# Optimization experiments

Measured on AMD Instinct MI355X. Metric: run time of the kernel, lower is better.

The kernel has to match this reference:

```python
import jax, jax.numpy as jnp
import numpy as np

B, T, E, H = 4, 512, 1024, 16
D = E // H  # 64
EPS = 1e-5  # torch LayerNorm default


def _ln(x, g, b):
    m = jnp.mean(x, axis=-1, keepdims=True)
    v = jnp.mean(jnp.square(x - m), axis=-1, keepdims=True)
    return (x - m) * jax.lax.rsqrt(v + EPS) * g + b


def _multihead(x, wq, wk, wv, g, b, mask):
    # x: [B,T,E]; wq/wk/wv: [H,E,D]; g,b: [H,D]; mask: [T,T] bool (causal)
    q = jnp.einsum('bte,hed->bhtd', x, wq)
    k = jnp.einsum('bte,hed->bhtd', x, wk)
    v = jnp.einsum('bte,hed->bhtd', x, wv)
    aff = jnp.einsum('bhtd,bhsd->bhts', q, k)  # NOTE: no 1/sqrt(d) scaling, as in source
    aff = jnp.where(mask, aff, -jnp.inf)
    p = jax.nn.softmax(aff, axis=-1)
    o = jnp.einsum('bhts,bhsd->bhtd', p, v)
    o = _ln(o, g[None, :, None, :], b[None, :, None, :])  # per-head LayerNorm over D
    o = o.transpose(0, 2, 1, 3).reshape(B, T, E)  # concat heads
    return x + o


def _ff(x, w1, b1, w2, b2, g, bb):
    h = jnp.maximum(jnp.einsum('bte,ef->btf', x, w1) + b1, 0.0)
    h = jnp.einsum('btf,fe->bte', h, w2) + b2
    h = _ln(h, g, bb)
    return x + h


def setup_inputs() -> dict:
    key = jax.random.key(0)
    ks = jax.random.split(key, 8)
    s = 0.02
    return {
        'x': jax.random.normal(ks[0], (B, T, E), jnp.float32),
        'mh_wq': jax.random.normal(ks[1], (5, H, E, D), jnp.float32) * s,
        'mh_wk': jax.random.normal(ks[2], (5, H, E, D), jnp.float32) * s,
        'mh_wv': jax.random.normal(ks[3], (5, H, E, D), jnp.float32) * s,
        'mh_g': jnp.ones((5, H, D), jnp.float32),
        'mh_b': jnp.zeros((5, H, D), jnp.float32),
        'ff_w1': jax.random.normal(ks[4], (4, E, 4 * E), jnp.float32) * s,
        'ff_b1': jnp.zeros((4, 4 * E), jnp.float32),
        'ff_w2': jax.random.normal(ks[5], (4, 4 * E, E), jnp.float32) * s,
        'ff_b2': jnp.zeros((4, E), jnp.float32),
        'ff_g': jnp.ones((4, E), jnp.float32),
        'ff_bb': jnp.zeros((4, E), jnp.float32),
        'lt_w': jax.random.normal(ks[6], (2 * E, E), jnp.float32) * s,
        'lt_b': jnp.zeros((E,), jnp.float32),
    }


def reference(x, mh_wq, mh_wk, mh_wv, mh_g, mh_b,
              ff_w1, ff_b1, ff_w2, ff_b2, ff_g, ff_bb, lt_w, lt_b):
    mask = jnp.tril(jnp.ones((T, T), dtype=bool))

    def mh(i, y):
        return _multihead(y, mh_wq[i], mh_wk[i], mh_wv[i], mh_g[i], mh_b[i], mask)

    def ff(i, y):
        return _ff(y, ff_w1[i], ff_b1[i], ff_w2[i], ff_b2[i], ff_g[i], ff_bb[i])

    def decoder(y):  # MultiHeadwithEncoder + FeedForward (param sets 4 / 3)
        return ff(3, mh(4, y))

    # head_one branch
    out_one = decoder(mh(0, x))
    # encoder branch: 3 EncoderBlocks (MultiHead + FeedForward each)
    out_two = x
    for i in range(3):
        out_two = ff(i, mh(1 + i, out_two))
    out_two = decoder(out_two)

    out = jnp.concatenate([out_one, out_two], axis=-1)
    out = jnp.einsum('btf,fe->bte', out, lt_w) + lt_b
    # input; the result is identical each time, so computing it once is faithful.
    return out
```

## Files before the change

### kernel.cpp

```cpp
#include <hip/hip_runtime.h>
#include <math.h>

#define Bb 4
#define Tt 512
#define Ee 1024
#define Hh 16
#define Dd 64
#define Ff 4096
#define Mm (Bb*Tt)
static constexpr float EPS = 1e-5f;

typedef __attribute__((ext_vector_type(4))) float f32x4;
typedef _Float16 f16;
typedef __attribute__((ext_vector_type(8))) _Float16 f16x8;

__device__ __forceinline__ void gload16(const void* g, void* l) {
  __builtin_amdgcn_global_load_lds(
      (const __attribute__((address_space(1))) unsigned int*)g,
      (__attribute__((address_space(3))) unsigned int*)l, 16, 0, 0);
}

__global__ __launch_bounds__(256)
void gemm_f16_128(const f16* __restrict__ A, const f16* __restrict__ W,
                  const float* __restrict__ bias,
                  f16* __restrict__ C, int ldc, int K)
{
  __shared__ f16 AS[128][32], BS[128][32];
  const int tid = threadIdx.x;
  const int lane = tid & 63, w = tid >> 6;
  const int wr = w >> 1, wc = w & 1;
  const int lhi = lane >> 4, llo = lane & 15;
  const int n0 = blockIdx.x * 128, m0 = blockIdx.y * 128;
  const int s_row = tid >> 2, s_ko = (tid & 3) * 8;

  f32x4 acc[4][4] = {};

  for (int k0 = 0; k0 < K; k0 += 32) {
#pragma unroll
    for (int i = 0; i < 2; ++i) {
      const int row = s_row + i * 64;
      gload16(&A[(size_t)(m0 + row) * K + k0 + s_ko], &AS[row][s_ko]);
      gload16(&W[(size_t)(n0 + row) * K + k0 + s_ko], &BS[row][s_ko]);
    }
    __syncthreads();
    f16x8 af[4], bf[4];
#pragma unroll
    for (int f = 0; f < 4; ++f) {
      af[f] = *(const f16x8*)&AS[wr * 64 + f * 16 + llo][lhi * 8];
      bf[f] = *(const f16x8*)&BS[wc * 64 + f * 16 + llo][lhi * 8];
    }
#pragma unroll
    for (int m = 0; m < 4; ++m)
#pragma unroll
      for (int n = 0; n < 4; ++n)
        acc[m][n] = __builtin_amdgcn_mfma_f32_16x16x32_f16(af[m], bf[n], acc[m][n], 0, 0, 0);
    __syncthreads();
  }

#pragma unroll
  for (int n = 0; n < 4; ++n) {
    const int col = n0 + wc * 64 + n * 16 + llo;
    const float bv = bias[col];
#pragma unroll
    for (int m = 0; m < 4; ++m) {
      const int rbase = m0 + wr * 64 + m * 16 + lhi * 4;
#pragma unroll
      for (int j = 0; j < 4; ++j) {
        float v = fmaxf(acc[m][n][j] + bv, 0.f);
        C[(size_t)(rbase + j) * ldc + col] = (f16)v;
      }
    }
  }
}

template<bool CONCAT>
__global__ __launch_bounds__(256)
void gemm_f16_1p(const f16* __restrict__ A, const f16* __restrict__ A2,
                 const f16* __restrict__ W,
                 float* __restrict__ Cf, float* __restrict__ Cf1,
                 int ldc, int K)
{
  __shared__ f16 AS[2][64][32], BS[2][128][32];
  const int tid = threadIdx.x;
  const int lane = tid & 63, w = tid >> 6;
  const int wr = w >> 1, wc = w & 1;
  const int lhi = lane >> 4, llo = lane & 15;
  const int n0 = blockIdx.x * 128;
  const int m0 = blockIdx.y * 64;
  const int half = K >> 1;
  const int kbeg = blockIdx.z * half;
  const int nt = half / 32;
  if (blockIdx.z == 1) Cf = Cf1;

  const int s_row = tid >> 2, s_ko = (tid & 3) * 8;

  auto stage = [&](int k0, int buf) {
    const int gk = k0 + s_ko;
    const f16* s = A;
    size_t g;
    if (CONCAT) {
      if (gk < Ee) { g = (size_t)(m0 + s_row) * Ee + gk; }
      else { g = (size_t)(m0 + s_row) * Ee + (gk - Ee); s = A2; }
    } else {
      g = (size_t)(m0 + s_row) * K + gk;
    }
    gload16(&s[g], &AS[buf][s_row][s_ko]);
#pragma unroll
    for (int i = 0; i < 2; ++i)
      gload16(&W[(size_t)(n0 + s_row + i * 64) * K + gk], &BS[buf][s_row + i * 64][s_ko]);
  };

  f32x4 acc[2][4] = {};
  stage(kbeg, 0);
  __syncthreads();
  int cur = 0;
  for (int t = 0; t < nt; ++t) {
    if (t + 1 < nt) stage(kbeg + (t + 1) * 32, cur ^ 1);
    f16x8 af[2], bf[4];
#pragma unroll
    for (int m = 0; m < 2; ++m)
      af[m] = *(const f16x8*)&AS[cur][wr * 32 + m * 16 + llo][lhi * 8];
#pragma unroll
    for (int n = 0; n < 4; ++n)
      bf[n] = *(const f16x8*)&BS[cur][wc * 64 + n * 16 + llo][lhi * 8];
#pragma unroll
    for (int m = 0; m < 2; ++m)
#pragma unroll
      for (int n = 0; n < 4; ++n)
        acc[m][n] = __builtin_amdgcn_mfma_f32_16x16x32_f16(af[m], bf[n], acc[m][n], 0, 0, 0);
    __syncthreads();
    cur ^= 1;
  }

#pragma unroll
  for (int n = 0; n < 4; ++n) {
    const int col = n0 + wc * 64 + n * 16 + llo;
#pragma unroll
    for (int m = 0; m < 2; ++m) {
      const int rbase = m0 + wr * 32 + m * 16 + lhi * 4;
#pragma unroll
      for (int j = 0; j < 4; ++j)
        Cf[(size_t)(rbase + j) * ldc + col] = acc[m][n][j];
    }
  }
}

__global__ __launch_bounds__(256)
void gemm_qkv(const f16* __restrict__ Ah_g, const f16* __restrict__ Al_g,
              const f16* __restrict__ Wh, const f16* __restrict__ Wl,
              f16* __restrict__ Qh, f16* __restrict__ Ql,
              f16* __restrict__ Kh, f16* __restrict__ Kl,
              f16* __restrict__ Vv)
{
  __shared__ f16 AhS[2][64][32], AlS[2][64][32];
  __shared__ f16 BhS[2][128][32], BlS[2][128][32];
  const int tid = threadIdx.x;
  const int lane = tid & 63, w = tid >> 6;
  const int wr = w >> 1, wc = w & 1;
  const int lhi = lane >> 4, llo = lane & 15;
  const int sec = blockIdx.x >> 3;
  const bool three = (sec < 2);
  const int n0 = (blockIdx.x & 7) * 128;
  Wh += (size_t)sec << 20;
  Wl += (size_t)sec << 20;
  const int m0 = blockIdx.y * 64;
  const int s_row = tid >> 2, s_ko = (tid & 3) * 8;

  auto stage = [&](int k0, int buf) {
    const size_t g = (size_t)(m0 + s_row) * Ee + k0 + s_ko;
    gload16(&Ah_g[g], &AhS[buf][s_row][s_ko]);
    if (three) gload16(&Al_g[g], &AlS[buf][s_row][s_ko]);
#pragma unroll
    for (int i = 0; i < 2; ++i) {
      size_t gb = (size_t)(n0 + s_row + i * 64) * Ee + k0 + s_ko;
      gload16(&Wh[gb], &BhS[buf][s_row + i * 64][s_ko]);
      if (three) gload16(&Wl[gb], &BlS[buf][s_row + i * 64][s_ko]);
    }
  };

  f32x4 acc[2][4] = {};
  stage(0, 0);
  __syncthreads();
  int cur = 0;
  for (int t = 0; t < Ee / 32; ++t) {
    if (t + 1 < Ee / 32) stage((t + 1) * 32, cur ^ 1);
    f16x8 ah[2], bh[4];
#pragma unroll
    for (int m = 0; m < 2; ++m)
      ah[m] = *(const f16x8*)&AhS[cur][wr * 32 + m * 16 + llo][lhi * 8];
#pragma unroll
    for (int n = 0; n < 4; ++n)
      bh[n] = *(const f16x8*)&BhS[cur][wc * 64 + n * 16 + llo][lhi * 8];
    if (three) {
      f16x8 al[2], bl[4];
#pragma unroll
      for (int m = 0; m < 2; ++m)
        al[m] = *(const f16x8*)&AlS[cur][wr * 32 + m * 16 + llo][lhi * 8];
#pragma unroll
      for (int n = 0; n < 4; ++n)
        bl[n] = *(const f16x8*)&BlS[cur][wc * 64 + n * 16 + llo][lhi * 8];
#pragma unroll
      for (int m = 0; m < 2; ++m)
#pragma unroll
        for (int n = 0; n < 4; ++n) {
          acc[m][n] = __builtin_amdgcn_mfma_f32_16x16x32_f16(ah[m], bh[n], acc[m][n], 0, 0, 0);
          acc[m][n] = __builtin_amdgcn_mfma_f32_16x16x32_f16(ah[m], bl[n], acc[m][n], 0, 0, 0);
          acc[m][n] = __builtin_amdgcn_mfma_f32_16x16x32_f16(al[m], bh[n], acc[m][n], 0, 0, 0);
        }
    } else {
#pragma unroll
      for (int m = 0; m < 2; ++m)
#pragma unroll
        for (int n = 0; n < 4; ++n)
          acc[m][n] = __builtin_amdgcn_mfma_f32_16x16x32_f16(ah[m], bh[n], acc[m][n], 0, 0, 0);
    }
    __syncthreads();
    cur ^= 1;
  }

#pragma unroll
  for (int n = 0; n < 4; ++n) {
    const int col = n0 + wc * 64 + n * 16 + llo;
#pragma unroll
    for (int m = 0; m < 2; ++m) {
      const int rbase = m0 + wr * 32 + m * 16 + lhi * 4;
#pragma unroll
      for (int j = 0; j < 4; ++j) {
        const float v = acc[m][n][j];
        const size_t idx = (size_t)(rbase + j) * Ee + col;
        if (sec == 0) {
          f16 h = (f16)v;
          Qh[idx] = h;
          Ql[idx] = (f16)(v - (float)h);
        } else if (sec == 1) {
          f16 h = (f16)v;
          Kh[idx] = h;
          Kl[idx] = (f16)(v - (float)h);
        } else {
          Vv[idx] = (f16)v;
        }
      }
    }
  }
}

__global__ __launch_bounds__(256)
void attn_ms(const f16* __restrict__ Qh_g, const f16* __restrict__ Ql_g,
             const f16* __restrict__ Kh_g, const f16* __restrict__ Kl_g,
             const f16* __restrict__ Vv_g, float* __restrict__ O)
{
  __shared__ f16 Ksh[64][72], Ksl[64][72];
  __shared__ f16 Vs[64][72];
  __shared__ f16 Pw[4][16][72];
  const int tid = threadIdx.x;
  const int lane = tid & 63, w = tid >> 6;
  const int lhi = lane >> 4, llo = lane & 15;
  const int q0 = blockIdx.x * 64;
  const int bh = blockIdx.y;
  const size_t base = (size_t)(bh >> 4) * Tt * Ee + (size_t)(bh & 15) * Dd;

  f16x8 qfh[2], qfl[2];
#pragma unroll
  for (int ks = 0; ks < 2; ++ks) {
    const size_t qoff = base + (size_t)(q0 + w * 16 + llo) * Ee + ks * 32 + lhi * 8;
    qfh[ks] = *(const f16x8*)&Qh_g[qoff];
    qfl[ks] = *(const f16x8*)&Ql_g[qoff];
  }

  f32x4 oacc[4] = {};
  float m_run[4], l_run[4];
#pragma unroll
  for (int j = 0; j < 4; ++j) { m_run[j] = -INFINITY; l_run[j] = 0.f; }

  for (int s0 = 0; s0 <= q0; s0 += 64) {
#pragma unroll
    for (int pass = 0; pass < 2; ++pass) {
      int c = tid + 256 * pass;
      int row = c >> 3, d0 = (c & 7) * 8;
      const size_t g = base + (size_t)(s0 + row) * Ee + d0;
      f16x8 kh = *(const f16x8*)&Kh_g[g];
      f16x8 kl = *(const f16x8*)&Kl_g[g];
      f16x8 vf = *(const f16x8*)&Vv_g[g];
      *(f16x8*)&Ksh[row][d0] = kh;
      *(f16x8*)&Ksl[row][d0] = kl;
#pragma unroll
      for (int j = 0; j < 8; ++j) Vs[d0 + j][row] = vf[j];
    }
    __syncthreads();

    f32x4 sacc[4] = {};
#pragma unroll
    for (int ks = 0; ks < 2; ++ks)
#pragma unroll
      for (int n = 0; n < 4; ++n) {
        f16x8 kfh = *(const f16x8*)&Ksh[n * 16 + llo][ks * 32 + lhi * 8];
        f16x8 kfl = *(const f16x8*)&Ksl[n * 16 + llo][ks * 32 + lhi * 8];
        sacc[n] = __builtin_amdgcn_mfma_f32_16x16x32_f16(qfh[ks], kfh, sacc[n], 0, 0, 0);
        sacc[n] = __builtin_amdgcn_mfma_f32_16x16x32_f16(qfh[ks], kfl, sacc[n], 0, 0, 0);
        sacc[n] = __builtin_amdgcn_mfma_f32_16x16x32_f16(qfl[ks], kfh, sacc[n], 0, 0, 0);
      }

    if (s0 == q0) {
#pragma unroll
      for (int n = 0; n < 4; ++n)
#pragma unroll
        for (int j = 0; j < 4; ++j)
          if (n * 16 + llo > w * 16 + lhi * 4 + j) sacc[n][j] = -INFINITY;
    }

    float scj[4];
#pragma unroll
    for (int j = 0; j < 4; ++j) {
      float mt = fmaxf(fmaxf(sacc[0][j], sacc[1][j]), fmaxf(sacc[2][j], sacc[3][j]));
#pragma unroll
      for (int off = 1; off < 16; off <<= 1) mt = fmaxf(mt, __shfl_xor(mt, off));
      float mn = fmaxf(m_run[j], mt);
      scj[j] = __expf(m_run[j] - mn);
      m_run[j] = mn;
      float rs = 0.f;
#pragma unroll
      for (int n = 0; n < 4; ++n) {
        float pp = __expf(sacc[n][j] - mn);
        sacc[n][j] = pp;
        rs += pp;
      }
#pragma unroll
      for (int off = 1; off < 16; off <<= 1) rs += __shfl_xor(rs, off);
      l_run[j] = l_run[j] * scj[j] + rs;
    }

#pragma unroll
    for (int n = 0; n < 4; ++n)
#pragma unroll
      for (int j = 0; j < 4; ++j)
        Pw[w][lhi * 4 + j][n * 16 + llo] = (f16)sacc[n][j];
#pragma unroll
    for (int df = 0; df < 4; ++df)
#pragma unroll
      for (int j = 0; j < 4; ++j)
        oacc[df][j] *= scj[j];

#pragma unroll
    for (int ks = 0; ks < 2; ++ks) {
      f16x8 pf = *(const f16x8*)&Pw[w][llo][ks * 32 + lhi * 8];
#pragma unroll
      for (int df = 0; df < 4; ++df) {
        f16x8 vfr = *(const f16x8*)&Vs[df * 16 + llo][ks * 32 + lhi * 8];
        oacc[df] = __builtin_amdgcn_mfma_f32_16x16x32_f16(pf, vfr, oacc[df], 0, 0, 0);
      }
    }
    __syncthreads();
  }

#pragma unroll
  for (int j = 0; j < 4; ++j) {
    float inv = 1.f / l_run[j];
#pragma unroll
    for (int df = 0; df < 4; ++df)
      O[base + (size_t)(q0 + w * 16 + lhi * 4 + j) * Ee + df * 16 + llo] =
          oacc[df][j] * inv;
  }
}

__global__ __launch_bounds__(256)
void attn_ln_res(const float* __restrict__ O, const float* Yin,
                 const float* __restrict__ g, const float* __restrict__ bta,
                 float* Yout, f16* __restrict__ Yh, f16* __restrict__ Yl)
{
  const int tid = threadIdx.x;
  const int w = (blockIdx.x << 2) + (tid >> 6);
  const int lane = tid & 63;
  const int m = w >> 4;
  const int h = w & 15;
  const size_t idx = (size_t)m * Ee + h * Dd + lane;
  float x = O[idx];
  float s = x, s2 = x * x;
#pragma unroll
  for (int off = 1; off < 64; off <<= 1) {
    s  += __shfl_xor(s, off);
    s2 += __shfl_xor(s2, off);
  }
  float mean = s * (1.f / 64.f);
  float var  = s2 * (1.f / 64.f) - mean * mean;
  float inv  = rsqrtf(var + EPS);
  float r = Yin[idx] + (x - mean) * inv * g[h * Dd + lane] + bta[h * Dd + lane];
  Yout[idx] = r;
  f16 hh = (f16)r;
  Yh[idx] = hh;
  Yl[idx] = (f16)(r - (float)hh);
}

__global__ __launch_bounds__(256)
void ff_ln_res(const float* __restrict__ T0, const float* __restrict__ T1,
               const float* __restrict__ b2,
               const float* Yin, const float* __restrict__ g,
               const float* __restrict__ bb,
               float* Yout, f16* __restrict__ Yh, f16* __restrict__ Yl)
{
  __shared__ float red[8];
  const int m = blockIdx.x;
  const int tid = threadIdx.x;
  const size_t basep = (size_t)m * Ee;
  float4 xa = *(const float4*)&T0[basep + (tid << 2)];
  float4 xb = *(const float4*)&T1[basep + (tid << 2)];
  float4 bv2 = *(const float4*)&b2[tid << 2];
  float xv[4] = {xa.x + xb.x + bv2.x, xa.y + xb.y + bv2.y,
                 xa.z + xb.z + bv2.z, xa.w + xb.w + bv2.w};
  float s  = xv[0] + xv[1] + xv[2] + xv[3];
  float s2 = xv[0]*xv[0] + xv[1]*xv[1] + xv[2]*xv[2] + xv[3]*xv[3];
#pragma unroll
  for (int off = 1; off < 64; off <<= 1) {
    s  += __shfl_xor(s, off);
    s2 += __shfl_xor(s2, off);
  }
  const int wid = tid >> 6;
  if ((tid & 63) == 0) { red[wid] = s; red[4 + wid] = s2; }
  __syncthreads();
  s  = red[0] + red[1] + red[2] + red[3];
  s2 = red[4] + red[5] + red[6] + red[7];
  float mean = s * (1.f / Ee);
  float var  = s2 * (1.f / Ee) - mean * mean;
  float inv  = rsqrtf(var + EPS);
  float4 y  = *(const float4*)&Yin[basep + (tid << 2)];
  float4 gg = *(const float4*)&g[tid << 2];
  float4 bv = *(const float4*)&bb[tid << 2];
  float gga[4] = {gg.x, gg.y, gg.z, gg.w};
  float bva[4] = {bv.x, bv.y, bv.z, bv.w};
  float ya[4] = {y.x, y.y, y.z, y.w};
  float o[4];
#pragma unroll
  for (int j = 0; j < 4; ++j) {
    o[j] = ya[j] + (xv[j] - mean) * inv * gga[j] + bva[j];
    f16 hh = (f16)o[j];
    Yh[basep + (tid << 2) + j] = hh;
    Yl[basep + (tid << 2) + j] = (f16)(o[j] - (float)hh);
  }
  *(float4*)&Yout[basep + (tid << 2)] = *(float4*)o;
}

__global__ __launch_bounds__(256)
void add2_bias(const float* __restrict__ p0, const float* __restrict__ p1,
               const float* __restrict__ b, float* __restrict__ out)
{
  const size_t i = ((size_t)blockIdx.x * 256 + threadIdx.x) * 4;
  const int col = (int)(i & (Ee - 1));
  float4 a = *(const float4*)&p0[i];
  float4 c = *(const float4*)&p1[i];
  float4 bb = *(const float4*)&b[col];
  float4 o;
  o.x = a.x + c.x + bb.x; o.y = a.y + c.y + bb.y;
  o.z = a.z + c.z + bb.z; o.w = a.w + c.w + bb.w;
  *(float4*)&out[i] = o;
}

__global__ __launch_bounds__(256)
void split_act2(const float* __restrict__ in,
                f16* __restrict__ oh1, f16* __restrict__ ol1,
                f16* __restrict__ oh2, f16* __restrict__ ol2)
{
  const size_t nb = gridDim.x >> 1;
  size_t bid = blockIdx.x;
  f16 *oh, *ol;
  if (bid < nb) { oh = oh1; ol = ol1; }
  else { bid -= nb; oh = oh2; ol = ol2; }
  const size_t i = (bid * 256 + threadIdx.x) * 4;
  float4 v = *(const float4*)&in[i];
  float f[4] = {v.x, v.y, v.z, v.w};
#pragma unroll
  for (int j = 0; j < 4; ++j) {
    f16 h = (f16)f[j];
    oh[i + j] = h;
    ol[i + j] = (f16)(f[j] - (float)h);
  }
}

__device__ __forceinline__ void cvtT_tile(const float* in, f16* outp,
                                          int R, int C, int tx, int ty, int tid)
{
  __shared__ float tile[64][33];
  const int c0 = tx * 32, r0 = ty * 64;
  const int r = tid >> 2, c8 = (tid & 3) * 8;
  const float* src = &in[(size_t)(r0 + r) * C + c0 + c8];
  float4 a = *(const float4*)src;
  float4 b = *(const float4*)(src + 4);
  tile[r][c8 + 0] = a.x; tile[r][c8 + 1] = a.y;
  tile[r][c8 + 2] = a.z; tile[r][c8 + 3] = a.w;
  tile[r][c8 + 4] = b.x; tile[r][c8 + 5] = b.y;
  tile[r][c8 + 6] = b.z; tile[r][c8 + 7] = b.w;
  __syncthreads();
  const int oc = tid >> 3, rr = (tid & 7) * 8;
  f16x8 o;
#pragma unroll
  for (int j = 0; j < 8; ++j) o[j] = (f16)tile[rr + j][oc];
  *(f16x8*)&outp[(size_t)(c0 + oc) * R + r0 + rr] = o;
}

__global__ __launch_bounds__(256)
void cvtT_f16(const float* __restrict__ in, f16* __restrict__ outp, int R, int C)
{
  const int nx = C >> 5;
  cvtT_tile(in, outp, R, C, blockIdx.x % nx, blockIdx.x / nx, threadIdx.x);
}

__global__ __launch_bounds__(256)
void cvtT_ff(const float* __restrict__ w1, const float* __restrict__ w2,
             f16* __restrict__ o1, f16* __restrict__ o2)
{
  constexpr int NT1 = (Ff / 32) * (Ee / 64);
  int id = blockIdx.x;
  const float* in; f16* outp; int R, C;
  if (id < NT1) { in = w1; outp = o1; R = Ee; C = Ff; }
  else { id -= NT1; in = w2; outp = o2; R = Ff; C = Ee; }
  const int nx = C >> 5;
  cvtT_tile(in, outp, R, C, id % nx, id / nx, threadIdx.x);
}

__global__ __launch_bounds__(256)
void cvtT_qkv(const float* __restrict__ wq, const float* __restrict__ wk,
              const float* __restrict__ wv, f16* __restrict__ out_h,
              f16* __restrict__ out_l)
{
  __shared__ float tile[64][33];
  const int z = blockIdx.z, sec = z >> 4, hh = z & 15;
  const float* in = (sec == 0) ? wq : (sec == 1) ? wk : wv;
  const size_t zi = (size_t)hh * Ee * Dd;
  const size_t zo = ((size_t)sec << 20) + (size_t)hh * Ee * Dd;
  const int c0 = blockIdx.x * 32, r0 = blockIdx.y * 64;
  const int tid = threadIdx.x;
  const int r = tid >> 2, c8 = (tid & 3) * 8;
  const float* src = &in[zi + (size_t)(r0 + r) * Dd + c0 + c8];
  float4 a = *(const float4*)src;
  float4 b = *(const float4*)(src + 4);
  tile[r][c8 + 0] = a.x; tile[r][c8 + 1] = a.y;
  tile[r][c8 + 2] = a.z; tile[r][c8 + 3] = a.w;
  tile[r][c8 + 4] = b.x; tile[r][c8 + 5] = b.y;
  tile[r][c8 + 6] = b.z; tile[r][c8 + 7] = b.w;
  __syncthreads();
  const int oc = tid >> 3, rr = (tid & 7) * 8;
  f16x8 oh, ol;
#pragma unroll
  for (int j = 0; j < 8; ++j) {
    float f = tile[rr + j][oc];
    f16 h = (f16)f;
    oh[j] = h;
    ol[j] = (f16)(f - (float)h);
  }
  const size_t ob = zo + (size_t)(c0 + oc) * Ee + r0 + rr;
  *(f16x8*)&out_h[ob] = oh;
  *(f16x8*)&out_l[ob] = ol;
}

extern "C" void kernel_launch(void* const* d_in, const int* in_sizes, int n_in,
                              void* d_out, int out_size, void* d_ws, size_t ws_size,
                              hipStream_t stream)
{
  const float* x     = (const float*)d_in[0];
  const float* mh_wq = (const float*)d_in[1];
  const float* mh_wk = (const float*)d_in[2];
  const float* mh_wv = (const float*)d_in[3];
  const float* mh_g  = (const float*)d_in[4];
  const float* mh_b  = (const float*)d_in[5];
  const float* ff_w1 = (const float*)d_in[6];
  const float* ff_b1 = (const float*)d_in[7];
  const float* ff_w2 = (const float*)d_in[8];
  const float* ff_b2 = (const float*)d_in[9];
  const float* ff_g  = (const float*)d_in[10];
  const float* ff_bb = (const float*)d_in[11];
  const float* lt_w  = (const float*)d_in[12];
  const float* lt_b  = (const float*)d_in[13];
  float* out = (float*)d_out;

  const size_t ME = (size_t)Mm * Ee;
  char* p = (char*)d_ws;
  auto alloc = [&](size_t bytes) { void* r = (void*)p; p += (bytes + 255) & ~(size_t)255; return r; };
  float* bufA  = (float*)alloc(ME * 4);
  f16*   bufAh = (f16*)alloc(ME * 2);
  f16*   bufAl = (f16*)alloc(ME * 2);
  float* bufB  = (float*)alloc(ME * 4);
  f16*   bufBh = (f16*)alloc(ME * 2);
  f16*   bufBl = (f16*)alloc(ME * 2);
  f16*   wt_h  = (f16*)alloc((size_t)Ff * Ee * 2);
  f16*   wt_l  = (f16*)alloc((size_t)Ff * Ee * 2);
  float* reg   = (float*)alloc((size_t)10 * 1024 * 1024 * 4);
  f16*   qh_   = (f16*)reg;
  f16*   ql_   = qh_ + ME;
  f16*   kh_   = qh_ + 2 * ME;
  f16*   kl_   = qh_ + 3 * ME;
  f16*   vv_   = qh_ + 4 * ME;
  float* ob    = reg + 5 * 1024 * 1024;
  f16*   hid   = (f16*)reg;
  float* tmp   = reg + 8 * 1024 * 1024;

  auto mh = [&](int i, const float* srcF, const f16* srcH, const f16* srcL,
                float* dstF, f16* dstH, f16* dstL) {
    const size_t wo = (size_t)i * Hh * Ee * Dd;
    cvtT_qkv<<<dim3(Dd / 32, Ee / 64, 48), 256, 0, stream>>>(
        mh_wq + wo, mh_wk + wo, mh_wv + wo, wt_h, wt_l);
    gemm_qkv<<<dim3(24, Mm / 64), 256, 0, stream>>>(
        srcH, srcL, wt_h, wt_l, qh_, ql_, kh_, kl_, vv_);
    attn_ms<<<dim3(Tt / 64, Bb * Hh), 256, 0, stream>>>(qh_, ql_, kh_, kl_, vv_, ob);
    attn_ln_res<<<dim3(Mm * Hh / 4), 256, 0, stream>>>(
        ob, srcF, mh_g + (size_t)i * Hh * Dd, mh_b + (size_t)i * Hh * Dd, dstF, dstH, dstL);
  };
  auto ff = [&](int i, const float* srcF, const f16* srcH,
                float* dstF, f16* dstH, f16* dstL, float* tmp1) {
    cvtT_ff<<<dim3((Ff / 32) * (Ee / 64) + (Ee / 32) * (Ff / 64)), 256, 0, stream>>>(
        ff_w1 + (size_t)i * Ee * Ff, ff_w2 + (size_t)i * Ff * Ee, wt_h, wt_l);
    gemm_f16_128<<<dim3(Ff / 128, Mm / 128), 256, 0, stream>>>(
        srcH, wt_h, ff_b1 + (size_t)i * Ff, hid, Ff, Ee);
    gemm_f16_1p<false><<<dim3(Ee / 128, Mm / 64, 2), 256, 0, stream>>>(
        hid, nullptr, wt_l, tmp, tmp1, Ee, Ff);
    ff_ln_res<<<dim3(Mm), 256, 0, stream>>>(
        tmp, tmp1, ff_b2 + (size_t)i * Ee,
        srcF, ff_g + (size_t)i * Ee, ff_bb + (size_t)i * Ee, dstF, dstH, dstL);
  };

  split_act2<<<dim3(2 * ME / 1024), 256, 0, stream>>>(x, bufAh, bufAl, bufBh, bufBl);

  mh(0, x, bufAh, bufAl, bufA, bufAh, bufAl);
  mh(4, bufA, bufAh, bufAl, bufA, bufAh, bufAl);
  ff(3, bufA, bufAh, bufA, bufAh, bufAl, bufB);

  mh(1, x, bufBh, bufBl, bufB, bufBh, bufBl);
  ff(0, bufB, bufBh, bufB, bufBh, bufBl, bufA);
  mh(2, bufB, bufBh, bufBl, bufB, bufBh, bufBl);
  ff(1, bufB, bufBh, bufB, bufBh, bufBl, bufA);
  mh(3, bufB, bufBh, bufBl, bufB, bufBh, bufBl);
  ff(2, bufB, bufBh, bufB, bufBh, bufBl, bufA);
  mh(4, bufB, bufBh, bufBl, bufB, bufBh, bufBl);
  ff(3, bufB, bufBh, bufB, bufBh, bufBl, bufA);

  cvtT_f16<<<dim3((Ee / 32) * (2 * Ee / 64)), 256, 0, stream>>>(lt_w, wt_h, 2 * Ee, Ee);
  gemm_f16_1p<true><<<dim3(Ee / 128, Mm / 64, 2), 256, 0, stream>>>(
      bufAh, bufBh, wt_h, bufA, bufB, Ee, 2 * Ee);
  add2_bias<<<dim3(ME / 1024), 256, 0, stream>>>(bufA, bufB, lt_b, out);
}
```

Baseline: 1.002 ms.

## Triple-buffer LDS staging in GEMM kernels with partial vmcnt waits

Result: slower. 1.152 ms (+15.0%).

```diff
diff --git a/kernel.cpp b/kernel.cpp
--- a/kernel.cpp
+++ b/kernel.cpp
@@ -19,13 +19,17 @@
       (const __attribute__((address_space(1))) unsigned int*)g,
       (__attribute__((address_space(3))) unsigned int*)l, 16, 0, 0);
 }
+__device__ __forceinline__ void wait_vm6() { asm volatile("s_waitcnt vmcnt(6)" ::: "memory"); }
+__device__ __forceinline__ void wait_vm4() { asm volatile("s_waitcnt vmcnt(4)" ::: "memory"); }
+__device__ __forceinline__ void wait_vm3() { asm volatile("s_waitcnt vmcnt(3)" ::: "memory"); }
+__device__ __forceinline__ void wait_vm0() { asm volatile("s_waitcnt vmcnt(0)" ::: "memory"); }
 
 __global__ __launch_bounds__(256)
 void gemm_f16_128(const f16* __restrict__ A, const f16* __restrict__ W,
                   const float* __restrict__ bias,
                   f16* __restrict__ C, int ldc, int K)
 {
-  __shared__ f16 AS[128][32], BS[128][32];
+  __shared__ f16 AS[3][128][32], BS[3][128][32];
   const int tid = threadIdx.x;
   const int lane = tid & 63, w = tid >> 6;
   const int wr = w >> 1, wc = w & 1;
@@ -33,28 +37,39 @@
   const int n0 = blockIdx.x * 128, m0 = blockIdx.y * 128;
   const int s_row = tid >> 2, s_ko = (tid & 3) * 8;
 
-  f32x4 acc[4][4] = {};
-
-  for (int k0 = 0; k0 < K; k0 += 32) {
+  auto stage = [&](int k0, int buf) {
 #pragma unroll
     for (int i = 0; i < 2; ++i) {
       const int row = s_row + i * 64;
-      gload16(&A[(size_t)(m0 + row) * K + k0 + s_ko], &AS[row][s_ko]);
-      gload16(&W[(size_t)(n0 + row) * K + k0 + s_ko], &BS[row][s_ko]);
-    }
-    __syncthreads();
+      gload16(&A[(size_t)(m0 + row) * K + k0 + s_ko], &AS[buf][row][s_ko]);
+      gload16(&W[(size_t)(n0 + row) * K + k0 + s_ko], &BS[buf][row][s_ko]);
+    }
+  };
+
+  f32x4 acc[4][4] = {};
+  const int nt = K / 32;
+  stage(0, 0);
+  stage(32, 1);
+  wait_vm4();
+  __builtin_amdgcn_s_barrier();
+  for (int t = 0; t < nt; ++t) {
+    const int cur = t % 3;
+    if (t + 2 < nt) stage((t + 2) * 32, (t + 2) % 3);
     f16x8 af[4], bf[4];
 #pragma unroll
     for (int f = 0; f < 4; ++f) {
-      af[f] = *(const f16x8*)&AS[wr * 64 + f * 16 + llo][lhi * 8];
-      bf[f] = *(const f16x8*)&BS[wc * 64 + f * 16 + llo][lhi * 8];
+      af[f] = *(const f16x8*)&AS[cur][wr * 64 + f * 16 + llo][lhi * 8];
+      bf[f] = *(const f16x8*)&BS[cur][wc * 64 + f * 16 + llo][lhi * 8];
     }
 #pragma unroll
     for (int m = 0; m < 4; ++m)
 #pragma unroll
       for (int n = 0; n < 4; ++n)
         acc[m][n] = __builtin_amdgcn_mfma_f32_16x16x32_f16(af[m], bf[n], acc[m][n], 0, 0, 0);
-    __syncthreads();
+    if (t + 1 < nt) {
+      if (t + 2 < nt) wait_vm4(); else wait_vm0();
+      __builtin_amdgcn_s_barrier();
+    }
   }
 
 #pragma unroll
@@ -80,7 +95,7 @@
                  float* __restrict__ Cf, float* __restrict__ Cf1,
                  int ldc, int K)
 {
-  __shared__ f16 AS[2][64][32], BS[2][128][32];
+  __shared__ f16 AS[3][64][32], BS[3][128][32];
   const int tid = threadIdx.x;
   const int lane = tid & 63, w = tid >> 6;
   const int wr = w >> 1, wc = w & 1;
@@ -112,10 +127,12 @@
 
   f32x4 acc[2][4] = {};
   stage(kbeg, 0);
-  __syncthreads();
-  int cur = 0;
+  stage(kbeg + 32, 1);
+  wait_vm3();
+  __builtin_amdgcn_s_barrier();
   for (int t = 0; t < nt; ++t) {
-    if (t + 1 < nt) stage(kbeg + (t + 1) * 32, cur ^ 1);
+    const int cur = t % 3;
+    if (t + 2 < nt) stage(kbeg + (t + 2) * 32, (t + 2) % 3);
     f16x8 af[2], bf[4];
 #pragma unroll
     for (int m = 0; m < 2; ++m)
@@ -128,8 +145,10 @@
 #pragma unroll
       for (int n = 0; n < 4; ++n)
         acc[m][n] = __builtin_amdgcn_mfma_f32_16x16x32_f16(af[m], bf[n], acc[m][n], 0, 0, 0);
-    __syncthreads();
-    cur ^= 1;
+    if (t + 1 < nt) {
+      if (t + 2 < nt) wait_vm3(); else wait_vm0();
+      __builtin_amdgcn_s_barrier();
+    }
   }
 
 #pragma unroll
@@ -152,8 +171,8 @@
               f16* __restrict__ Kh, f16* __restrict__ Kl,
               f16* __restrict__ Vv)
 {
-  __shared__ f16 AhS[2][64][32], AlS[2][64][32];
-  __shared__ f16 BhS[2][128][32], BlS[2][128][32];
+  __shared__ f16 AhS[3][64][32], AlS[3][64][32];
+  __shared__ f16 BhS[3][128][32], BlS[3][128][32];
   const int tid = threadIdx.x;
   const int lane = tid & 63, w = tid >> 6;
   const int wr = w >> 1, wc = w & 1;
@@ -177,13 +196,17 @@
       if (three) gload16(&Wl[gb], &BlS[buf][s_row + i * 64][s_ko]);
     }
   };
+  auto wait_vmL = [&]() { if (three) wait_vm6(); else wait_vm3(); };
 
   f32x4 acc[2][4] = {};
+  constexpr int nt = Ee / 32;
   stage(0, 0);
-  __syncthreads();
-  int cur = 0;
-  for (int t = 0; t < Ee / 32; ++t) {
-    if (t + 1 < Ee / 32) stage((t + 1) * 32, cur ^ 1);
+  stage(32, 1);
+  wait_vmL();
+  __builtin_amdgcn_s_barrier();
+  for (int t = 0; t < nt; ++t) {
+    const int cur = t % 3;
+    if (t + 2 < nt) stage((t + 2) * 32, (t + 2) % 3);
     f16x8 ah[2], bh[4];
 #pragma unroll
     for (int m = 0; m < 2; ++m)
@@ -214,8 +237,10 @@
         for (int n = 0; n < 4; ++n)
           acc[m][n] = __builtin_amdgcn_mfma_f32_16x16x32_f16(ah[m], bh[n], acc[m][n], 0, 0, 0);
     }
-    __syncthreads();
-    cur ^= 1;
+    if (t + 1 < nt) {
+      if (t + 2 < nt) wait_vmL(); else wait_vm0();
+      __builtin_amdgcn_s_barrier();
+    }
   }
 
 #pragma unroll
```
